# Optimization experiments

Hardware: AMD Instinct MI355X
Metric: run time of the kernel (lower is better)

## Reference

```python
import jax, jax.numpy as jnp
import numpy as np

B, T, C = 4, 2048, 1024
N_HEAD = 16
HEAD_DIM = C // N_HEAD
SCALE = 1.0 / np.sqrt(HEAD_DIM).astype(np.float32)


def setup_inputs() -> dict:
    key = jax.random.key(0)
    k1, k2, k3 = jax.random.split(key, 3)
    x = jax.random.normal(k1, (B, T, C), dtype=jnp.float32)
    # torch Linear weights: [out_features, in_features], scaled init
    w_qkv = jax.random.normal(k2, (3 * C, C), dtype=jnp.float32) * (1.0 / np.sqrt(C))
    w_out = jax.random.normal(k3, (C, C), dtype=jnp.float32) * (1.0 / np.sqrt(C))
    b_out = jnp.zeros((C,), dtype=jnp.float32)
    return {"x": x, "w_qkv": w_qkv, "w_out": w_out, "b_out": b_out}


def reference(x, w_qkv, w_out, b_out):
    Bsz, Tlen, Cdim = x.shape
    qkv = jnp.einsum('btc,oc->bto', x, w_qkv)  # [B,T,3C]
    q, k, v = jnp.split(qkv, 3, axis=-1)
    # [B,H,T,D]
    def heads(t):
        return t.reshape(Bsz, Tlen, N_HEAD, HEAD_DIM).transpose(0, 2, 1, 3)
    q, k, v = heads(q), heads(k), heads(v)
    att = jnp.einsum('bhqd,bhkd->bhqk', q, k) * SCALE  # [B,H,T,T]
    causal = jnp.tril(jnp.ones((Tlen, Tlen), dtype=bool))
    att = jnp.where(causal[None, None], att, -jnp.inf)
    att = jax.nn.softmax(att, axis=-1)
    out = jnp.einsum('bhqk,bhkd->bhqd', att, v)
    out = out.transpose(0, 2, 1, 3).reshape(Bsz, Tlen, Cdim)
    out = jnp.einsum('btc,oc->bto', out, w_out) + b_out
    return out
```

## Files before the change

kernel.cpp:

```cpp
#include <hip/hip_runtime.h>
#include <stdint.h>


typedef __attribute__((ext_vector_type(8))) short bf16x8;
typedef __attribute__((ext_vector_type(4))) float f32x4;

#define EXP2F(x) __builtin_amdgcn_exp2f(x)
#define SL2E 0.18033688011112042f
#define FIXED_M 15.0f

__device__ __forceinline__ short f2bf(float f) {
  union { float f; unsigned u; } c; c.f = f;
  unsigned u = c.u;
  unsigned r = (u + 0x7fffu + ((u >> 16) & 1u)) >> 16;
  return (short)(unsigned short)r;
}

__device__ __forceinline__ short f2bf_trunc(float f) {
  union { float f; unsigned u; } c; c.f = f;
  return (short)(unsigned short)(c.u >> 16);
}

__device__ __forceinline__ void llds16(const short* g, short* l) {
  __builtin_amdgcn_global_load_lds(
      (const __attribute__((address_space(1))) unsigned int*)g,
      (__attribute__((address_space(3))) unsigned int*)l, 16, 0, 0);
}

__global__ __launch_bounds__(256) void cast_f32_to_bf16(
    const float* __restrict__ src, short* __restrict__ dst, int n4) {
  int i = blockIdx.x * 256 + threadIdx.x;
  if (i >= n4) return;
  float4 f = ((const float4*)src)[i];
  short4 o;
  o.x = f2bf(f.x); o.y = f2bf(f.y); o.z = f2bf(f.z); o.w = f2bf(f.w);
  ((short4*)dst)[i] = o;
}

__global__ __launch_bounds__(256) void gemm_qkv(
    const short* __restrict__ A, const short* __restrict__ Bw,
    short* __restrict__ Qo, short* __restrict__ Ko, short* __restrict__ Vt) {
  const int K = 1024;
  __shared__ short smem[17408];
  short* lA = smem;
  short* lB = smem + 8192;
  const int tid = threadIdx.x;
  const int lane = tid & 63;
  const int wave = tid >> 6;
  const int m0 = blockIdx.y * 128;
  const int n0 = blockIdx.x * 128;
  const int wm = (wave >> 1) * 64;
  const int wn = (wave & 1) * 64;
  const int mrow = lane & 15;
  const int kq = lane >> 4;

  f32x4 acc[4][4];
#pragma unroll
  for (int i = 0; i < 4; ++i)
#pragma unroll
    for (int j = 0; j < 4; ++j) acc[i][j] = (f32x4){0.f, 0.f, 0.f, 0.f};

  for (int k0 = 0; k0 < K; k0 += 64) {
#pragma unroll
    for (int call = 0; call < 4; ++call) {
      const int cb = call * 256 + wave * 64;
      const int c = cb + lane;
      const int row = c >> 3;
      const int scol = (c & 7) ^ (row & 7);
      llds16(A + (size_t)(m0 + row) * K + k0 + scol * 8, &lA[cb * 8]);
      llds16(Bw + (size_t)(n0 + row) * K + k0 + scol * 8, &lB[cb * 8]);
    }
    __syncthreads();
#pragma unroll
    for (int kk = 0; kk < 2; ++kk) {
      bf16x8 af[4], bfr[4];
#pragma unroll
      for (int i = 0; i < 4; ++i) {
        const int row = wm + i * 16 + mrow;
        af[i] = *(const bf16x8*)&lA[row * 64 + (((kk * 4 + kq) ^ (row & 7)) * 8)];
      }
#pragma unroll
      for (int j = 0; j < 4; ++j) {
        const int row = wn + j * 16 + mrow;
        bfr[j] = *(const bf16x8*)&lB[row * 64 + (((kk * 4 + kq) ^ (row & 7)) * 8)];
      }
#pragma unroll
      for (int i = 0; i < 4; ++i)
#pragma unroll
        for (int j = 0; j < 4; ++j)
          acc[i][j] = __builtin_amdgcn_mfma_f32_16x16x32_bf16(af[i], bfr[j], acc[i][j], 0, 0, 0);
    }
    __syncthreads();
  }

  const int b = m0 >> 11;
  if (n0 < 2048) {
    short* lC = smem;
#pragma unroll
    for (int i = 0; i < 4; ++i) {
      const int row = wm + i * 16 + kq * 4;
#pragma unroll
      for (int j = 0; j < 4; ++j) {
        const int col = wn + j * 16 + mrow;
        const float sc_ = (((n0 + col) >> 10) == 1) ? SL2E : 1.0f;
#pragma unroll
        for (int r = 0; r < 4; ++r)
          lC[(row + r) * 132 + col] = f2bf(acc[i][j][r] * sc_);
      }
    }
    __syncthreads();
#pragma unroll
    for (int call = 0; call < 8; ++call) {
      const int cc = call * 256 + tid;
      const int row = cc >> 4;
      const int t = (m0 + row) & 2047;
      const int o = n0 + (cc & 15) * 8;
      const int c = o & 1023;
      const int h = c >> 6;
      const int d = c & 63;
      short* dst = (o >> 10) == 0 ? Qo : Ko;
      bf16x8 val = *(const bf16x8*)&lC[row * 132 + (cc & 15) * 8];
      *(bf16x8*)(dst + ((size_t)(b * 16 + h) * 2048 + t) * 64 + d) = val;
    }
  } else {
    short* lCt = smem;
#pragma unroll
    for (int i = 0; i < 4; ++i) {
      const int row = wm + i * 16 + kq * 4;
#pragma unroll
      for (int j = 0; j < 4; ++j) {
        const int col = wn + j * 16 + mrow;
#pragma unroll
        for (int r = 0; r < 4; ++r)
          lCt[col * 136 + row + r] = f2bf(acc[i][j][r]);
      }
    }
    __syncthreads();
#pragma unroll
    for (int call = 0; call < 8; ++call) {
      const int cc = call * 256 + tid;
      const int col = cc >> 4;
      const int tg = cc & 15;
      const int o = n0 + col;
      const int d = o & 63;
      const int h = (o >> 6) & 15;
      const int t = (m0 & 2047) + tg * 8;
      bf16x8 val = *(const bf16x8*)&lCt[col * 136 + tg * 8];
      *(bf16x8*)(Vt + ((size_t)(b * 16 + h) * 64 + d) * 2048 + t) = val;
    }
  }
}

__global__ __launch_bounds__(256) void gemm_out(
    const short* __restrict__ A, const short* __restrict__ Bw,
    const float* __restrict__ bias, float* __restrict__ Out) {
  const int K = 1024;
  __shared__ short lA[128 * 64];
  __shared__ short lB[128 * 64];
  const int tid = threadIdx.x;
  const int lane = tid & 63;
  const int wave = tid >> 6;
  const int m0 = blockIdx.y * 128;
  const int n0 = blockIdx.x * 128;
  const int wm = (wave >> 1) * 64;
  const int wn = (wave & 1) * 64;
  const int mrow = lane & 15;
  const int kq = lane >> 4;

  f32x4 acc[4][4];
#pragma unroll
  for (int i = 0; i < 4; ++i)
#pragma unroll
    for (int j = 0; j < 4; ++j) acc[i][j] = (f32x4){0.f, 0.f, 0.f, 0.f};

  for (int k0 = 0; k0 < K; k0 += 64) {
#pragma unroll
    for (int call = 0; call < 4; ++call) {
      const int cb = call * 256 + wave * 64;
      const int c = cb + lane;
      const int row = c >> 3;
      const int scol = (c & 7) ^ (row & 7);
      llds16(A + (size_t)(m0 + row) * K + k0 + scol * 8, &lA[cb * 8]);
      llds16(Bw + (size_t)(n0 + row) * K + k0 + scol * 8, &lB[cb * 8]);
    }
    __syncthreads();
#pragma unroll
    for (int kk = 0; kk < 2; ++kk) {
      bf16x8 af[4], bfr[4];
#pragma unroll
      for (int i = 0; i < 4; ++i) {
        const int row = wm + i * 16 + mrow;
        af[i] = *(const bf16x8*)&lA[row * 64 + (((kk * 4 + kq) ^ (row & 7)) * 8)];
      }
#pragma unroll
      for (int j = 0; j < 4; ++j) {
        const int row = wn + j * 16 + mrow;
        bfr[j] = *(const bf16x8*)&lB[row * 64 + (((kk * 4 + kq) ^ (row & 7)) * 8)];
      }
#pragma unroll
      for (int i = 0; i < 4; ++i)
#pragma unroll
        for (int j = 0; j < 4; ++j)
          acc[i][j] = __builtin_amdgcn_mfma_f32_16x16x32_bf16(af[i], bfr[j], acc[i][j], 0, 0, 0);
    }
    __syncthreads();
  }

#pragma unroll
  for (int i = 0; i < 4; ++i) {
    const int m = m0 + wm + i * 16 + kq * 4;
#pragma unroll
    for (int j = 0; j < 4; ++j) {
      const int n = n0 + wn + j * 16 + mrow;
      const float bb = bias[n];
#pragma unroll
      for (int r = 0; r < 4; ++r)
        Out[(size_t)(m + r) * 1024 + n] = acc[i][j][r] + bb;
    }
  }
}

__global__ __launch_bounds__(256) void flash_attn(
    const short* __restrict__ Qg, const short* __restrict__ Kg,
    const short* __restrict__ Vtg, short* __restrict__ Og) {
  const int T = 2048;
  __shared__ short lK[2][64 * 64];
  __shared__ short lVt[2][64 * 64];
  __shared__ short lP[4 * 16 * 76];
  const int tid = threadIdx.x;
  const int lane = tid & 63;
  const int wave = tid >> 6;
  const int bh = blockIdx.x;
  const int mrow = lane & 15;
  const int kq = lane >> 4;
  const int swz = mrow & 7;
  const size_t base = (size_t)bh * T * 64;
  const size_t vbase = (size_t)bh * 64 * T;
  const int qtA = blockIdx.y;
  const int qtB = 31 - qtA;

  const bf16x8 ones = {0x3F80, 0x3F80, 0x3F80, 0x3F80, 0x3F80, 0x3F80, 0x3F80, 0x3F80};

  bf16x8 aqA0, aqA1, aqB0, aqB1;
  {
    const short* qpA = Qg + base + (size_t)(qtA * 64 + wave * 16 + mrow) * 64 + kq * 8;
    aqA0 = *(const bf16x8*)qpA;
    aqA1 = *(const bf16x8*)(qpA + 32);
    const short* qpB = Qg + base + (size_t)(qtB * 64 + wave * 16 + mrow) * 64 + kq * 8;
    aqB0 = *(const bf16x8*)qpB;
    aqB1 = *(const bf16x8*)(qpB + 32);
  }

  f32x4 accA[4], accB[4], lacA, lacB;
#pragma unroll
  for (int jd = 0; jd < 4; ++jd) {
    accA[jd] = (f32x4){0.f, 0.f, 0.f, 0.f};
    accB[jd] = (f32x4){0.f, 0.f, 0.f, 0.f};
  }
  lacA = (f32x4){0.f, 0.f, 0.f, 0.f};
  lacB = (f32x4){0.f, 0.f, 0.f, 0.f};

  auto stage = [&](int nt, int buf) {
#pragma unroll
    for (int call = 0; call < 2; ++call) {
      const int cb = call * 256 + wave * 64;
      const int c = cb + lane;
      const int row = c >> 3;
      const int scol = (c & 7) ^ (row & 7);
      llds16(Kg + base + (size_t)(nt * 64 + row) * 64 + scol * 8, &lK[buf][cb * 8]);
      llds16(Vtg + vbase + (size_t)row * T + nt * 64 + scol * 8, &lVt[buf][cb * 8]);
    }
  };

  stage(0, 0);
  __syncthreads();

  for (int kt = 0; kt <= qtB; ++kt) {
    const int bcur = kt & 1;
    if (kt < qtB) stage(kt + 1, bcur ^ 1);
    const short* K_ = lK[bcur];
    const short* Vt_ = lVt[bcur];

    auto seg_compute = [&](int qt, bf16x8 aq0, bf16x8 aq1, f32x4* acc, f32x4& lac) {
      f32x4 sc[4];
#pragma unroll
      for (int j = 0; j < 4; ++j) {
        const short* krow = &K_[(j * 16 + mrow) * 64];
        bf16x8 kb0 = *(const bf16x8*)&krow[(kq ^ swz) * 8];
        bf16x8 kb1 = *(const bf16x8*)&krow[((4 + kq) ^ swz) * 8];
        f32x4 s = (f32x4){-FIXED_M, -FIXED_M, -FIXED_M, -FIXED_M};
        s = __builtin_amdgcn_mfma_f32_16x16x32_bf16(aq0, kb0, s, 0, 0, 0);
        s = __builtin_amdgcn_mfma_f32_16x16x32_bf16(aq1, kb1, s, 0, 0, 0);
        sc[j] = s;
      }

      if (kt == qt) {
        const int qrow = qt * 64 + wave * 16 + kq * 4;
#pragma unroll
        for (int j = 0; j < 4; ++j) {
          const int key = kt * 64 + j * 16 + mrow;
#pragma unroll
          for (int r = 0; r < 4; ++r)
            if (key > qrow + r) sc[j][r] = -1e30f;
        }
      }

      short* pw = &lP[wave * 1216];
#pragma unroll
      for (int j = 0; j < 4; ++j)
#pragma unroll
        for (int r = 0; r < 4; ++r)
          pw[(kq * 4 + r) * 76 + j * 16 + mrow] = f2bf_trunc(EXP2F(sc[j][r]));

      bf16x8 pa0 = *(const bf16x8*)&lP[wave * 1216 + mrow * 76 + kq * 8];
      bf16x8 pa1 = *(const bf16x8*)&lP[wave * 1216 + mrow * 76 + 32 + kq * 8];
      lac = __builtin_amdgcn_mfma_f32_16x16x32_bf16(pa0, ones, lac, 0, 0, 0);
      lac = __builtin_amdgcn_mfma_f32_16x16x32_bf16(pa1, ones, lac, 0, 0, 0);
#pragma unroll
      for (int jd = 0; jd < 4; ++jd) {
        const short* vrow = &Vt_[(jd * 16 + mrow) * 64];
        bf16x8 vb0 = *(const bf16x8*)&vrow[(kq ^ swz) * 8];
        bf16x8 vb1 = *(const bf16x8*)&vrow[((4 + kq) ^ swz) * 8];
        acc[jd] = __builtin_amdgcn_mfma_f32_16x16x32_bf16(pa0, vb0, acc[jd], 0, 0, 0);
        acc[jd] = __builtin_amdgcn_mfma_f32_16x16x32_bf16(pa1, vb1, acc[jd], 0, 0, 0);
      }
    };

    if (kt <= qtA) seg_compute(qtA, aqA0, aqA1, accA, lacA);
    seg_compute(qtB, aqB0, aqB1, accB, lacB);
    __syncthreads();
  }

  const int b = bh >> 4;
  const int h = bh & 15;
#pragma unroll
  for (int r = 0; r < 4; ++r) {
    const float invA = 1.0f / lacA[r];
    const float invB = 1.0f / lacB[r];
    const int tA = qtA * 64 + wave * 16 + kq * 4 + r;
    const int tB = qtB * 64 + wave * 16 + kq * 4 + r;
#pragma unroll
    for (int jd = 0; jd < 4; ++jd) {
      const int col = h * 64 + jd * 16 + mrow;
      Og[((size_t)b * 2048 + tA) * 1024 + col] = f2bf(accA[jd][r] * invA);
      Og[((size_t)b * 2048 + tB) * 1024 + col] = f2bf(accB[jd][r] * invB);
    }
  }
}

extern "C" void kernel_launch(void* const* d_in, const int* in_sizes, int n_in,
                              void* d_out, int out_size, void* d_ws, size_t ws_size,
                              hipStream_t stream) {
  const float* x = (const float*)d_in[0];
  const float* w_qkv = (const float*)d_in[1];
  const float* w_out = (const float*)d_in[2];
  const float* b_out = (const float*)d_in[3];
  float* out = (float*)d_out;

  char* ws = (char*)d_ws;
  const size_t NX = 8192ull * 1024;
  const size_t NWQ = 3072ull * 1024;
  const size_t NWO = 1024ull * 1024;
  const size_t NQ = 64ull * 2048 * 64;
  size_t off = 0;
  short* xb    = (short*)(ws + off); off += NX * 2;
  short* wqkvb = (short*)(ws + off); off += NWQ * 2;
  short* woutb = (short*)(ws + off); off += NWO * 2;
  short* q     = (short*)(ws + off); off += NQ * 2;
  short* k     = (short*)(ws + off); off += NQ * 2;
  short* vt    = (short*)(ws + off); off += NQ * 2;
  short* attb  = (short*)(ws + off); off += NX * 2;
  if (off > ws_size) return;

  cast_f32_to_bf16<<<(int)(NX / 4 / 256), 256, 0, stream>>>(x, xb, (int)(NX / 4));
  cast_f32_to_bf16<<<(int)(NWQ / 4 / 256), 256, 0, stream>>>(w_qkv, wqkvb, (int)(NWQ / 4));
  cast_f32_to_bf16<<<(int)(NWO / 4 / 256), 256, 0, stream>>>(w_out, woutb, (int)(NWO / 4));
  gemm_qkv<<<dim3(24, 64), 256, 0, stream>>>(xb, wqkvb, q, k, vt);
  flash_attn<<<dim3(64, 16), 256, 0, stream>>>(q, k, vt, attb);
  gemm_out<<<dim3(8, 64), 256, 0, stream>>>(attb, woutb, b_out, out);
}
```

Before: 262.7 us.

## Double-buffer GEMM K-loops and process four query tiles per attention block

```diff
diff --git a/kernel.cpp b/kernel.cpp
--- a/kernel.cpp
+++ b/kernel.cpp
@@ -42,8 +42,6 @@
     short* __restrict__ Qo, short* __restrict__ Ko, short* __restrict__ Vt) {
   const int K = 1024;
   __shared__ short smem[17408];
-  short* lA = smem;
-  short* lB = smem + 8192;
   const int tid = threadIdx.x;
   const int lane = tid & 63;
   const int wave = tid >> 6;
@@ -60,36 +58,44 @@
 #pragma unroll
     for (int j = 0; j < 4; ++j) acc[i][j] = (f32x4){0.f, 0.f, 0.f, 0.f};
 
-  for (int k0 = 0; k0 < K; k0 += 64) {
-#pragma unroll
-    for (int call = 0; call < 4; ++call) {
+  auto stage = [&](int it, int buf) {
+#pragma unroll
+    for (int call = 0; call < 2; ++call) {
       const int cb = call * 256 + wave * 64;
       const int c = cb + lane;
-      const int row = c >> 3;
-      const int scol = (c & 7) ^ (row & 7);
-      llds16(A + (size_t)(m0 + row) * K + k0 + scol * 8, &lA[cb * 8]);
-      llds16(Bw + (size_t)(n0 + row) * K + k0 + scol * 8, &lB[cb * 8]);
-    }
-    __syncthreads();
-#pragma unroll
-    for (int kk = 0; kk < 2; ++kk) {
-      bf16x8 af[4], bfr[4];
-#pragma unroll
-      for (int i = 0; i < 4; ++i) {
-        const int row = wm + i * 16 + mrow;
-        af[i] = *(const bf16x8*)&lA[row * 64 + (((kk * 4 + kq) ^ (row & 7)) * 8)];
-      }
-#pragma unroll
-      for (int j = 0; j < 4; ++j) {
-        const int row = wn + j * 16 + mrow;
-        bfr[j] = *(const bf16x8*)&lB[row * 64 + (((kk * 4 + kq) ^ (row & 7)) * 8)];
-      }
-#pragma unroll
-      for (int i = 0; i < 4; ++i)
-#pragma unroll
-        for (int j = 0; j < 4; ++j)
-          acc[i][j] = __builtin_amdgcn_mfma_f32_16x16x32_bf16(af[i], bfr[j], acc[i][j], 0, 0, 0);
-    }
+      const int row = c >> 2;
+      const int scol = (c & 3) ^ (row & 3);
+      llds16(A + (size_t)(m0 + row) * K + it * 32 + scol * 8,
+             &smem[buf * 8192 + cb * 8]);
+      llds16(Bw + (size_t)(n0 + row) * K + it * 32 + scol * 8,
+             &smem[buf * 8192 + 4096 + cb * 8]);
+    }
+  };
+
+  stage(0, 0);
+  __syncthreads();
+
+  for (int it = 0; it < 32; ++it) {
+    const int buf = it & 1;
+    if (it < 31) stage(it + 1, buf ^ 1);
+    const short* lA = &smem[buf * 8192];
+    const short* lB = &smem[buf * 8192 + 4096];
+    bf16x8 af[4], bfr[4];
+#pragma unroll
+    for (int i = 0; i < 4; ++i) {
+      const int row = wm + i * 16 + mrow;
+      af[i] = *(const bf16x8*)&lA[row * 32 + ((kq ^ (row & 3)) * 8)];
+    }
+#pragma unroll
+    for (int j = 0; j < 4; ++j) {
+      const int row = wn + j * 16 + mrow;
+      bfr[j] = *(const bf16x8*)&lB[row * 32 + ((kq ^ (row & 3)) * 8)];
+    }
+#pragma unroll
+    for (int i = 0; i < 4; ++i)
+#pragma unroll
+      for (int j = 0; j < 4; ++j)
+        acc[i][j] = __builtin_amdgcn_mfma_f32_16x16x32_bf16(af[i], bfr[j], acc[i][j], 0, 0, 0);
     __syncthreads();
   }
 
@@ -155,8 +161,7 @@
     const short* __restrict__ A, const short* __restrict__ Bw,
     const float* __restrict__ bias, float* __restrict__ Out) {
   const int K = 1024;
-  __shared__ short lA[128 * 64];
-  __shared__ short lB[128 * 64];
+  __shared__ short smem[16384];
   const int tid = threadIdx.x;
   const int lane = tid & 63;
   const int wave = tid >> 6;
@@ -173,36 +178,44 @@
 #pragma unroll
     for (int j = 0; j < 4; ++j) acc[i][j] = (f32x4){0.f, 0.f, 0.f, 0.f};
 
-  for (int k0 = 0; k0 < K; k0 += 64) {
-#pragma unroll
-    for (int call = 0; call < 4; ++call) {
+  auto stage = [&](int it, int buf) {
+#pragma unroll
+    for (int call = 0; call < 2; ++call) {
       const int cb = call * 256 + wave * 64;
       const int c = cb + lane;
-      const int row = c >> 3;
-      const int scol = (c & 7) ^ (row & 7);
-      llds16(A + (size_t)(m0 + row) * K + k0 + scol * 8, &lA[cb * 8]);
-      llds16(Bw + (size_t)(n0 + row) * K + k0 + scol * 8, &lB[cb * 8]);
-    }
-    __syncthreads();
-#pragma unroll
-    for (int kk = 0; kk < 2; ++kk) {
-      bf16x8 af[4], bfr[4];
-#pragma unroll
-      for (int i = 0; i < 4; ++i) {
-        const int row = wm + i * 16 + mrow;
-        af[i] = *(const bf16x8*)&lA[row * 64 + (((kk * 4 + kq) ^ (row & 7)) * 8)];
-      }
-#pragma unroll
-      for (int j = 0; j < 4; ++j) {
-        const int row = wn + j * 16 + mrow;
-        bfr[j] = *(const bf16x8*)&lB[row * 64 + (((kk * 4 + kq) ^ (row & 7)) * 8)];
-      }
-#pragma unroll
-      for (int i = 0; i < 4; ++i)
-#pragma unroll
-        for (int j = 0; j < 4; ++j)
-          acc[i][j] = __builtin_amdgcn_mfma_f32_16x16x32_bf16(af[i], bfr[j], acc[i][j], 0, 0, 0);
-    }
+      const int row = c >> 2;
+      const int scol = (c & 3) ^ (row & 3);
+      llds16(A + (size_t)(m0 + row) * K + it * 32 + scol * 8,
+             &smem[buf * 8192 + cb * 8]);
+      llds16(Bw + (size_t)(n0 + row) * K + it * 32 + scol * 8,
+             &smem[buf * 8192 + 4096 + cb * 8]);
+    }
+  };
+
+  stage(0, 0);
+  __syncthreads();
+
+  for (int it = 0; it < 32; ++it) {
+    const int buf = it & 1;
+    if (it < 31) stage(it + 1, buf ^ 1);
+    const short* lA = &smem[buf * 8192];
+    const short* lB = &smem[buf * 8192 + 4096];
+    bf16x8 af[4], bfr[4];
+#pragma unroll
+    for (int i = 0; i < 4; ++i) {
+      const int row = wm + i * 16 + mrow;
+      af[i] = *(const bf16x8*)&lA[row * 32 + ((kq ^ (row & 3)) * 8)];
+    }
+#pragma unroll
+    for (int j = 0; j < 4; ++j) {
+      const int row = wn + j * 16 + mrow;
+      bfr[j] = *(const bf16x8*)&lB[row * 32 + ((kq ^ (row & 3)) * 8)];
+    }
+#pragma unroll
+    for (int i = 0; i < 4; ++i)
+#pragma unroll
+      for (int j = 0; j < 4; ++j)
+        acc[i][j] = __builtin_amdgcn_mfma_f32_16x16x32_bf16(af[i], bfr[j], acc[i][j], 0, 0, 0);
     __syncthreads();
   }
 
@@ -231,34 +244,36 @@
   const int lane = tid & 63;
   const int wave = tid >> 6;
   const int bh = blockIdx.x;
+  const int bx = blockIdx.y;
   const int mrow = lane & 15;
   const int kq = lane >> 4;
   const int swz = mrow & 7;
   const size_t base = (size_t)bh * T * 64;
   const size_t vbase = (size_t)bh * 64 * T;
-  const int qtA = blockIdx.y;
-  const int qtB = 31 - qtA;
+
+  int qts[4];
+  qts[0] = bx;
+  qts[1] = 31 - bx;
+  qts[2] = 15 - bx;
+  qts[3] = 16 + bx;
 
   const bf16x8 ones = {0x3F80, 0x3F80, 0x3F80, 0x3F80, 0x3F80, 0x3F80, 0x3F80, 0x3F80};
 
-  bf16x8 aqA0, aqA1, aqB0, aqB1;
-  {
-    const short* qpA = Qg + base + (size_t)(qtA * 64 + wave * 16 + mrow) * 64 + kq * 8;
-    aqA0 = *(const bf16x8*)qpA;
-    aqA1 = *(const bf16x8*)(qpA + 32);
-    const short* qpB = Qg + base + (size_t)(qtB * 64 + wave * 16 + mrow) * 64 + kq * 8;
-    aqB0 = *(const bf16x8*)qpB;
-    aqB1 = *(const bf16x8*)(qpB + 32);
-  }
-
-  f32x4 accA[4], accB[4], lacA, lacB;
-#pragma unroll
-  for (int jd = 0; jd < 4; ++jd) {
-    accA[jd] = (f32x4){0.f, 0.f, 0.f, 0.f};
-    accB[jd] = (f32x4){0.f, 0.f, 0.f, 0.f};
-  }
-  lacA = (f32x4){0.f, 0.f, 0.f, 0.f};
-  lacB = (f32x4){0.f, 0.f, 0.f, 0.f};
+  bf16x8 aq0[4], aq1[4];
+#pragma unroll
+  for (int s = 0; s < 4; ++s) {
+    const short* qp = Qg + base + (size_t)(qts[s] * 64 + wave * 16 + mrow) * 64 + kq * 8;
+    aq0[s] = *(const bf16x8*)qp;
+    aq1[s] = *(const bf16x8*)(qp + 32);
+  }
+
+  f32x4 acc[4][4], lac[4];
+#pragma unroll
+  for (int s = 0; s < 4; ++s) {
+    lac[s] = (f32x4){0.f, 0.f, 0.f, 0.f};
+#pragma unroll
+    for (int jd = 0; jd < 4; ++jd) acc[s][jd] = (f32x4){0.f, 0.f, 0.f, 0.f};
+  }
 
   auto stage = [&](int nt, int buf) {
 #pragma unroll
@@ -275,23 +290,28 @@
   stage(0, 0);
   __syncthreads();
 
-  for (int kt = 0; kt <= qtB; ++kt) {
+  const int ktmax = qts[1];
+  for (int kt = 0; kt <= ktmax; ++kt) {
     const int bcur = kt & 1;
-    if (kt < qtB) stage(kt + 1, bcur ^ 1);
+    if (kt < ktmax) stage(kt + 1, bcur ^ 1);
     const short* K_ = lK[bcur];
     const short* Vt_ = lVt[bcur];
 
-    auto seg_compute = [&](int qt, bf16x8 aq0, bf16x8 aq1, f32x4* acc, f32x4& lac) {
+#pragma unroll
+    for (int s = 0; s < 4; ++s) {
+      const int qt = qts[s];
+      if (kt > qt) continue;
+
       f32x4 sc[4];
 #pragma unroll
       for (int j = 0; j < 4; ++j) {
         const short* krow = &K_[(j * 16 + mrow) * 64];
         bf16x8 kb0 = *(const bf16x8*)&krow[(kq ^ swz) * 8];
         bf16x8 kb1 = *(const bf16x8*)&krow[((4 + kq) ^ swz) * 8];
-        f32x4 s = (f32x4){-FIXED_M, -FIXED_M, -FIXED_M, -FIXED_M};
-        s = __builtin_amdgcn_mfma_f32_16x16x32_bf16(aq0, kb0, s, 0, 0, 0);
-        s = __builtin_amdgcn_mfma_f32_16x16x32_bf16(aq1, kb1, s, 0, 0, 0);
-        sc[j] = s;
+        f32x4 ss = (f32x4){-FIXED_M, -FIXED_M, -FIXED_M, -FIXED_M};
+        ss = __builtin_amdgcn_mfma_f32_16x16x32_bf16(aq0[s], kb0, ss, 0, 0, 0);
+        ss = __builtin_amdgcn_mfma_f32_16x16x32_bf16(aq1[s], kb1, ss, 0, 0, 0);
+        sc[j] = ss;
       }
 
       if (kt == qt) {
@@ -314,36 +334,33 @@
 
       bf16x8 pa0 = *(const bf16x8*)&lP[wave * 1216 + mrow * 76 + kq * 8];
       bf16x8 pa1 = *(const bf16x8*)&lP[wave * 1216 + mrow * 76 + 32 + kq * 8];
-      lac = __builtin_amdgcn_mfma_f32_16x16x32_bf16(pa0, ones, lac, 0, 0, 0);
-      lac = __builtin_amdgcn_mfma_f32_16x16x32_bf16(pa1, ones, lac, 0, 0, 0);
+      lac[s] = __builtin_amdgcn_mfma_f32_16x16x32_bf16(pa0, ones, lac[s], 0, 0, 0);
+      lac[s] = __builtin_amdgcn_mfma_f32_16x16x32_bf16(pa1, ones, lac[s], 0, 0, 0);
 #pragma unroll
       for (int jd = 0; jd < 4; ++jd) {
         const short* vrow = &Vt_[(jd * 16 + mrow) * 64];
         bf16x8 vb0 = *(const bf16x8*)&vrow[(kq ^ swz) * 8];
         bf16x8 vb1 = *(const bf16x8*)&vrow[((4 + kq) ^ swz) * 8];
-        acc[jd] = __builtin_amdgcn_mfma_f32_16x16x32_bf16(pa0, vb0, acc[jd], 0, 0, 0);
-        acc[jd] = __builtin_amdgcn_mfma_f32_16x16x32_bf16(pa1, vb1, acc[jd], 0, 0, 0);
-      }
-    };
-
-    if (kt <= qtA) seg_compute(qtA, aqA0, aqA1, accA, lacA);
-    seg_compute(qtB, aqB0, aqB1, accB, lacB);
+        acc[s][jd] = __builtin_amdgcn_mfma_f32_16x16x32_bf16(pa0, vb0, acc[s][jd], 0, 0, 0);
+        acc[s][jd] = __builtin_amdgcn_mfma_f32_16x16x32_bf16(pa1, vb1, acc[s][jd], 0, 0, 0);
+      }
+    }
     __syncthreads();
   }
 
   const int b = bh >> 4;
   const int h = bh & 15;
 #pragma unroll
-  for (int r = 0; r < 4; ++r) {
-    const float invA = 1.0f / lacA[r];
-    const float invB = 1.0f / lacB[r];
-    const int tA = qtA * 64 + wave * 16 + kq * 4 + r;
-    const int tB = qtB * 64 + wave * 16 + kq * 4 + r;
-#pragma unroll
-    for (int jd = 0; jd < 4; ++jd) {
-      const int col = h * 64 + jd * 16 + mrow;
-      Og[((size_t)b * 2048 + tA) * 1024 + col] = f2bf(accA[jd][r] * invA);
-      Og[((size_t)b * 2048 + tB) * 1024 + col] = f2bf(accB[jd][r] * invB);
+  for (int s = 0; s < 4; ++s) {
+#pragma unroll
+    for (int r = 0; r < 4; ++r) {
+      const float inv = 1.0f / lac[s][r];
+      const int t = qts[s] * 64 + wave * 16 + kq * 4 + r;
+#pragma unroll
+      for (int jd = 0; jd < 4; ++jd) {
+        const int col = h * 64 + jd * 16 + mrow;
+        Og[((size_t)b * 2048 + t) * 1024 + col] = f2bf(acc[s][jd][r] * inv);
+      }
     }
   }
 }
@@ -376,6 +393,6 @@
   cast_f32_to_bf16<<<(int)(NWQ / 4 / 256), 256, 0, stream>>>(w_qkv, wqkvb, (int)(NWQ / 4));
   cast_f32_to_bf16<<<(int)(NWO / 4 / 256), 256, 0, stream>>>(w_out, woutb, (int)(NWO / 4));
   gemm_qkv<<<dim3(24, 64), 256, 0, stream>>>(xb, wqkvb, q, k, vt);
-  flash_attn<<<dim3(64, 16), 256, 0, stream>>>(q, k, vt, attb);
+  flash_attn<<<dim3(64, 8), 256, 0, stream>>>(q, k, vt, attb);
   gemm_out<<<dim3(8, 64), 256, 0, stream>>>(attb, woutb, b_out, out);
 }
```

New measurement: 261.6 us. About the same (-0.4%).
